# Kernel tuning notes

Measured on AMD Instinct MI355X. Metric: run time of the kernel, lower is better.

## Reference

```python
import jax, jax.numpy as jnp
import numpy as np

SR = 48000.0


def _lin_interp(x, n):
    # Matches torch F.interpolate(mode='linear', align_corners=False) on last axis.
    T = x.shape[-1]
    pos = (jnp.arange(n, dtype=jnp.float32) + 0.5) * (T / n) - 0.5
    pos = jnp.clip(pos, 0.0, T - 1)
    i0 = jnp.floor(pos).astype(jnp.int32)
    i1 = jnp.minimum(i0 + 1, T - 1)
    w = (pos - i0.astype(jnp.float32)).astype(x.dtype)
    return jnp.take(x, i0, axis=-1) * (1.0 - w) + jnp.take(x, i1, axis=-1) * w


def setup_inputs() -> dict:
    key = jax.random.key(0)
    k1, k2, k3 = jax.random.split(key, 3)
    B, T, N = 16, 250, 100
    harm_amps = jax.random.uniform(k1, (B, T, N), dtype=jnp.float32)
    # realistic fundamental frequencies: 80..480 Hz
    f0_hz = 80.0 + 400.0 * jax.random.uniform(k2, (B, T), dtype=jnp.float32)
    # small inharmonicity coefficients (piano-like): ~0..1e-4
    inh = 1e-4 * jax.random.uniform(k3, (B,), dtype=jnp.float32)
    return {"harm_amps": harm_amps, "f0_hz": f0_hz, "inh": inh, "n_samples": 48000}


def reference(harm_amps, f0_hz, inh, n_samples):
    B, T, N = harm_amps.shape
    # upsample amplitudes (B,N,n_samples) and f0 (B,n_samples)
    a = _lin_interp(jnp.transpose(harm_amps, (0, 2, 1)), n_samples)
    f0_up = _lin_interp(f0_hz, n_samples)
    k = jnp.arange(1, N + 1, dtype=jnp.float32)  # harmonic numbers 1..N
    stretch = jnp.sqrt(1.0 + inh[:, None] * k ** 2)  # (B,N)
    inst_freq = f0_up[:, None, :] * (k[None, :] * stretch)[:, :, None]  # (B,N,n)
    nyq_mask = (inst_freq < SR * 0.45).astype(a.dtype)
    phase = jnp.cumsum(2.0 * jnp.pi * inst_freq / SR, axis=-1)
    signal = jnp.sum(a * nyq_mask * jnp.sin(phase), axis=1, keepdims=True)  # (B,1,n)
    return signal / N
```

## Files before the change

### kernel.cpp

```cpp
#include <hip/hip_runtime.h>
#include <cmath>

#pragma clang fp contract(off)

#define SRF   48000.0f
#define NYQF  21600.0f
constexpr float  TWO_PI_F  = 6.283185307179586476925286766559f;
constexpr double INV_2PI_D = 0.15915494309189533576888376337251;
constexpr float  RC1 = (float)INV_2PI_D;
constexpr float  RC2 = (float)(INV_2PI_D - (double)RC1);
constexpr double INV_SR_D = 1.0 / 48000.0;
constexpr float  DD1 = (float)INV_SR_D;
constexpr float  DD2 = (float)(INV_SR_D - (double)DD1);

__device__ __forceinline__ float hsin_rev(float r) {
#if __has_builtin(__builtin_amdgcn_sinf)
    return __builtin_amdgcn_sinf(r);
#else
    return __sinf(r * TWO_PI_F);
#endif
}

__device__ __forceinline__ float div48000(float t) {
    float h = t * DD1;
    float r = __builtin_fmaf(t, DD1, -h);
    float s = __builtin_fmaf(t, DD2, r);
    return h + s;
}

__device__ __forceinline__ float sin_phase(float ph) {
    float h  = ph * RC1;
    float r  = __builtin_fmaf(ph, RC1, -h);
    float s  = __builtin_fmaf(ph, RC2, r);
    float nn = __builtin_rintf(h);
    float fr = (h - nn) + s;
    return hsin_rev(fr);
}

template <int IDX>
__device__ __forceinline__ float grp4_bcast(float v, int lb) {
#if __has_builtin(__builtin_amdgcn_ds_swizzle)
    constexpr int imm = (IDX << 5) | 0x1C;
    return __int_as_float(__builtin_amdgcn_ds_swizzle(__float_as_int(v), imm));
#else
    return __shfl(v, lb + IDX);
#endif
}

__device__ __forceinline__ float kcval(int k, float ib) {
    float kf = (float)(k + 1);
    float k2 = kf * kf;
    float m  = ib * k2;
    float s1 = 1.0f + m;
    float st = (float)sqrt((double)s1);
    return kf * st;
}

__global__ void __launch_bounds__(256) k_f0up(const float* __restrict__ f0,
        float* __restrict__ f0up, float* __restrict__ out,
        int T, int n, float pf) {
    int j = blockIdx.x * 256 + threadIdx.x;
    int b = blockIdx.y;
    if (j >= n) return;
    float pos = ((float)j + 0.5f);
    pos = pos * pf;
    pos = pos - 0.5f;
    pos = fmaxf(pos, 0.0f);
    pos = fminf(pos, (float)(T - 1));
    int   i0 = (int)pos;
    int   i1 = min(i0 + 1, T - 1);
    float w  = pos - (float)i0;
    float omw = 1.0f - w;
    const float* fb = f0 + b * T;
    f0up[(size_t)b * n + j] = fb[i0] * omw + fb[i1] * w;
    out[(size_t)b * n + j]  = 0.0f;
}

__global__ void __launch_bounds__(256) k_scan4(const float* __restrict__ f0up,
        const float* __restrict__ inh, float* __restrict__ scan4,
        int N, int n) {
    __shared__ float lv[6016];
    const int k   = blockIdx.x;
    const int b   = blockIdx.y;
    const int tid = threadIdx.x;
    const float kc = kcval(k, inh[b]);
    const float4* f4 = (const float4*)(f0up + (size_t)b * n);
    const int len4 = n >> 4;

    auto l2of = [&](float4 v) -> float {
        float a0 = div48000(TWO_PI_F * (kc * v.x));
        float a1 = div48000(TWO_PI_F * (kc * v.y));
        float a2 = div48000(TWO_PI_F * (kc * v.z));
        float a3 = div48000(TWO_PI_F * (kc * v.w));
        return (a0 + a1) + (a2 + a3);
    };
    for (int i = tid; i < len4; i += 256) {
        float s01 = l2of(f4[4*i])     + l2of(f4[4*i + 1]);
        float s23 = l2of(f4[4*i + 2]) + l2of(f4[4*i + 3]);
        lv[i] = s01 + s23;
    }
    __syncthreads();

    int offp = 0, lenp = len4, P = 4;
    for (int l = 5; ; ++l) {
        int lenc = lenp >> 1;
        int offc = offp + lenp;
        for (int i = tid; i < lenc; i += 256)
            lv[offc + i] = lv[offp + 2*i] + lv[offp + 2*i + 1];
        __syncthreads();
        P = l;
        if (lenc == 1) break;
        offp = offc; lenp = lenc;
    }
    for (int l = P - 1; l >= 4; --l) {
        int lenl = n >> l;
        int offl = 0;
        for (int m = 4; m < l; ++m) offl += (n >> m);
        int offh = offl + lenl;
        int lenh = n >> (l + 1);
        float*       arr = lv + offl;
        const float* hi  = lv + offh;
        for (int i = tid; i < lenh; i += 256) {
            float v = hi[i];
            int e = 2*i + 2;
            if (e < lenl) arr[e] = v + arr[e];
            arr[2*i + 1] = v;
        }
        __syncthreads();
    }
    float* sp = scan4 + (size_t)(b * N + k) * (len4 + 1);
    if (tid == 0) sp[0] = 0.0f;
    for (int i = tid; i < len4; i += 256) sp[1 + i] = lv[i];
}

__global__ void __launch_bounds__(256) k_synth4(
        const float* __restrict__ harm, const float* __restrict__ f0up,
        const float* __restrict__ inh,  const float* __restrict__ scan4,
        float* __restrict__ out, int B, int T, int N, int n, float pf, int kpg) {
    const int tid  = threadIdx.x;
    const int b    = blockIdx.y;
    const int k0   = blockIdx.z * kpg;
    const int g    = blockIdx.x * 256 + tid;
    const int q    = g >> 2;
    const int c    = g & 3;
    const int NG   = n >> 4;
    const int NGP  = NG + 1;
    const int kend = min(k0 + kpg, N);
    const int kact = kend - k0;
    const bool valid = q < NG;

    __shared__ float2 amps[8 * 32];
    __shared__ float  kcs[32];

    const float ib    = inh[b];
    const float tmaxf = (float)(T - 1);
    for (int i = tid; i < kact; i += 256) kcs[i] = kcval(k0 + i, ib);

    const int j0blk = blockIdx.x * 1024;
    int i0min;
    {
        float p = ((float)j0blk + 0.5f);
        p = p * pf; p = p - 0.5f;
        p = fmaxf(p, 0.0f); p = fminf(p, tmaxf);
        i0min = (int)p;
    }
    for (int idx = tid; idx < 8 * kact; idx += 256) {
        int r = idx / kact, kk = idx - r * kact;
        int r0 = min(i0min + r, T - 1);
        int r1 = min(i0min + r + 1, T - 1);
        float a0 = harm[((size_t)b * T + r0) * N + (k0 + kk)];
        float a1 = harm[((size_t)b * T + r1) * N + (k0 + kk)];
        amps[idx] = make_float2(a0, a1 - a0);
    }
    __syncthreads();

    float u0=0.f,u1=0.f,u2=0.f,u3=0.f;
    float w0=0.f,w1=0.f,w2=0.f,w3=0.f;
    int   a0o=0,a1o=0,a2o=0,a3o=0;
    float um = __builtin_inff();
    if (valid) {
        const float4 v = *(const float4*)(f0up + (size_t)b * n + (size_t)q * 16 + c * 4);
        u0=v.x; u1=v.y; u2=v.z; u3=v.w;
        um = fminf(fminf(u0,u1), fminf(u2,u3));
        const int jb = q * 16 + c * 4;
        #pragma unroll
        for (int i = 0; i < 4; ++i) {
            float p = ((float)(jb + i) + 0.5f);
            p = p * pf; p = p - 0.5f;
            p = fmaxf(p, 0.0f); p = fminf(p, tmaxf);
            int i0 = (int)p;
            float wv = p - (float)i0;
            int aoo  = (i0 - i0min) * kact;
            if (i==0){w0=wv;a0o=aoo;}
            else if (i==1){w1=wv;a1o=aoo;}
            else if (i==2){w2=wv;a2o=aoo;}
            else {w3=wv;a3o=aoo;}
        }
    }
    #pragma unroll
    for (int off = 32; off > 0; off >>= 1)
        um = fminf(um, __shfl_xor(um, off));
    const float umin = um;
    const int lb = (tid & 63) & ~3;

    if (valid) {
        float acc0=0.f, acc1=0.f, acc2=0.f, acc3=0.f;
        const float* s4k = scan4 + (size_t)(b * N + k0) * NGP;
        float g0c = s4k[q];
        float g1c = s4k[q + 1];

        for (int k = k0; k < kend; ++k) {
            const int   kk = k - k0;
            const float kc = kcs[kk];
            if (kc * umin >= NYQF) break;
            const float G0 = g0c, G1 = g1c;
            if (k + 1 < kend) {
                const float* nx = s4k + NGP;
                g0c = nx[q];
                g1c = nx[q + 1];
                s4k = nx;
            }

            float x0 = div48000(TWO_PI_F * (kc * u0));
            float x1 = div48000(TWO_PI_F * (kc * u1));
            float x2 = div48000(TWO_PI_F * (kc * u2));
            float x3 = div48000(TWO_PI_F * (kc * u3));
            float L1p = x0 + x1, L1q = x2 + x3;
            float L2  = L1p + L1q;

            float s0 = grp4_bcast<0>(L2, lb);
            float s1 = grp4_bcast<1>(L2, lb);
            float s2 = grp4_bcast<2>(L2, lb);
            float t01 = s0 + s1;
            float b1v = G0 + s0;
            float b2v = G0 + t01;
            float b3v = b2v + s2;
            float base = (c == 0) ? G0  : (c == 1) ? b1v : (c == 2) ? b2v : b3v;
            float bn   = (c == 0) ? b1v : (c == 1) ? b2v : (c == 2) ? b3v : G1;

            float ph0 = base + x0;
            float ph1 = base + L1p;
            float ph2 = ph1 + x2;
            float ph3 = bn;

            {   float t1 = kc * u0;
                if (t1 < NYQF) { float sv = sin_phase(ph0);
                    float2 a = amps[a0o + kk];
                    acc0 = __builtin_fmaf(__builtin_fmaf(w0, a.y, a.x), sv, acc0); } }
            {   float t1 = kc * u1;
                if (t1 < NYQF) { float sv = sin_phase(ph1);
                    float2 a = amps[a1o + kk];
                    acc1 = __builtin_fmaf(__builtin_fmaf(w1, a.y, a.x), sv, acc1); } }
            {   float t1 = kc * u2;
                if (t1 < NYQF) { float sv = sin_phase(ph2);
                    float2 a = amps[a2o + kk];
                    acc2 = __builtin_fmaf(__builtin_fmaf(w2, a.y, a.x), sv, acc2); } }
            {   float t1 = kc * u3;
                if (t1 < NYQF) { float sv = sin_phase(ph3);
                    float2 a = amps[a3o + kk];
                    acc3 = __builtin_fmaf(__builtin_fmaf(w3, a.y, a.x), sv, acc3); } }
        }

        const float Nf = (float)N;
        float* ob = out + (size_t)b * n + (size_t)q * 16 + c * 4;
        atomicAdd(&ob[0], acc0 / Nf);
        atomicAdd(&ob[1], acc1 / Nf);
        atomicAdd(&ob[2], acc2 / Nf);
        atomicAdd(&ob[3], acc3 / Nf);
    }
}

__global__ void __launch_bounds__(256) k_scan_synth(
        const float* __restrict__ harm, const float* __restrict__ f0up,
        const float* __restrict__ inh,  float* __restrict__ out,
        int B, int T, int N, int n, float pf) {
    extern __shared__ float lv[];
    const int k   = blockIdx.x;
    const int b   = blockIdx.y;
    const int tid = threadIdx.x;
    const float kc = kcval(k, inh[b]);
    const float* fb = f0up + (size_t)b * n;

    auto inc = [&](int j) -> float {
        float u    = fb[j];
        float inst = kc * u;
        float tt   = TWO_PI_F * inst;
        return tt / SRF;
    };

    const int len1 = n >> 1;
    {
        const float4* f4 = (const float4*)fb;
        for (int i = tid; i < (n >> 2); i += 256) {
            float4 u = f4[i];
            float a0 = (TWO_PI_F * (kc * u.x)) / SRF;
            float a1 = (TWO_PI_F * (kc * u.y)) / SRF;
            float a2 = (TWO_PI_F * (kc * u.z)) / SRF;
            float a3 = (TWO_PI_F * (kc * u.w)) / SRF;
            lv[i] = (a0 + a1) + (a2 + a3);
        }
    }
    __syncthreads();
    int offp = 0, lenp = n >> 2, P = 2;
    for (int l = 3; ; ++l) {
        int lenc = lenp >> 1;
        int offc = offp + lenp;
        for (int i = tid; i < lenc; i += 256)
            lv[offc + i] = lv[offp + 2*i] + lv[offp + 2*i + 1];
        __syncthreads();
        P = l;
        if (lenc == 1) break;
        offp = offc; lenp = lenc;
    }
    for (int l = P - 1; l >= 2; --l) {
        int lenl = n >> l;
        int offl = 0;
        for (int m = 2; m < l; ++m) offl += (n >> m);
        float*       arr = lv + offl;
        const float* hi  = lv + offl + lenl;
        int lenh = n >> (l + 1);
        for (int i = tid; i < lenh; i += 256) {
            float v = hi[i];
            int e = 2*i + 2;
            if (e < lenl) arr[e] = v + arr[e];
            arr[2*i + 1] = v;
        }
        __syncthreads();
    }
    const float* scan2 = lv;

    const float  tmaxf = (float)(T - 1);
    const float  invN  = 1.0f / (float)N;
    const float* hb    = harm + (size_t)b * T * N + k;
    float*       ob    = out + (size_t)b * n;

    auto emit = [&](int j, float ph) {
        float u    = fb[j];
        float inst = kc * u;
        if (!(inst < NYQF)) return;
        double pr = (double)ph * INV_2PI_D;
        double fr = pr - rint(pr);
        float  sv = hsin_rev((float)fr);
        float pos = ((float)j + 0.5f);
        pos = pos * pf; pos = pos - 0.5f;
        pos = fmaxf(pos, 0.0f); pos = fminf(pos, tmaxf);
        int   i0 = (int)pos;
        int   i1 = min(i0 + 1, T - 1);
        float w  = pos - (float)i0;
        float a  = hb[(size_t)i0 * N] * (1.0f - w) + hb[(size_t)i1 * N] * w;
        atomicAdd(&ob[j], (a * sv) * invN);
    };

    if (tid == 0) emit(0, inc(0));
    for (int tt = tid; tt < len1; tt += 256) {
        float s1;
        if (tt == 0)      s1 = inc(0) + inc(1);
        else if (tt & 1)  s1 = scan2[(tt - 1) >> 1];
        else              s1 = scan2[(tt >> 1) - 1] + (inc(2*tt) + inc(2*tt + 1));
        emit(2*tt + 1, s1);
        int je = 2*tt + 2;
        if (je < n) emit(je, s1 + inc(je));
    }
}

extern "C" void kernel_launch(void* const* d_in, const int* in_sizes, int n_in,
                              void* d_out, int out_size, void* d_ws, size_t ws_size,
                              hipStream_t stream) {
    const int B = in_sizes[2];
    const int T = in_sizes[1] / B;
    const int N = in_sizes[0] / (B * T);
    const int n = out_size / B;
    const float pf = (float)((double)T / (double)n);

    const float* harm = (const float*)d_in[0];
    const float* f0   = (const float*)d_in[1];
    const float* inh  = (const float*)d_in[2];
    float* out  = (float*)d_out;
    float* f0up = (float*)d_ws;

    const int KZ  = 4;
    const int kpg = (N + KZ - 1) / KZ;
    const int NG  = n / 16;
    const size_t needFast = (size_t)B * n * 4 + (size_t)B * N * (NG + 1) * 4;
    const bool fast = (ws_size >= needFast) && (n % 16 == 0) && (kpg <= 32);

    k_f0up<<<dim3((n + 255) / 256, B), 256, 0, stream>>>(f0, f0up, out, T, n, pf);

    if (fast) {
        float* scan4 = (float*)((char*)d_ws + (size_t)B * n * 4);
        k_scan4<<<dim3(N, B), 256, 0, stream>>>(f0up, inh, scan4, N, n);
        const int tiles = (NG * 4 + 255) / 256;
        k_synth4<<<dim3(tiles, B, KZ), 256, 0, stream>>>(
            harm, f0up, inh, scan4, out, B, T, N, n, pf, kpg);
    } else {
        const size_t lds_bytes = (size_t)(n / 2) * sizeof(float);
        k_scan_synth<<<dim3(N, B), 256, lds_bytes, stream>>>(
            harm, f0up, inh, out, B, T, N, n, pf);
    }
}
```

Before: 153.0 us.

## Process eight samples per thread in synth kernel with pairwise phase broadcast

The synthesis kernel now has each thread handle 8 consecutive samples instead of 4, so a 16-sample group is split across 2 lanes rather than 4. The intra-group phase prefix needs only one even-lane swizzle broadcast instead of three, and per-sample Nyquist branches become predicated selects. Each block now covers 2048 samples with a larger amplitude tile in shared memory, and a host-side guard keeps that tile within bounds. The trade-off is more registers per thread and half as many threads in the grid.

```diff
diff --git a/kernel.cpp b/kernel.cpp
--- a/kernel.cpp
+++ b/kernel.cpp
@@ -37,13 +37,11 @@
     return hsin_rev(fr);
 }
 
-template <int IDX>
-__device__ __forceinline__ float grp4_bcast(float v, int lb) {
+__device__ __forceinline__ float pair_bcast_even(float v, int lane) {
 #if __has_builtin(__builtin_amdgcn_ds_swizzle)
-    constexpr int imm = (IDX << 5) | 0x1C;
-    return __int_as_float(__builtin_amdgcn_ds_swizzle(__float_as_int(v), imm));
+    return __int_as_float(__builtin_amdgcn_ds_swizzle(__float_as_int(v), 0x001E));
 #else
-    return __shfl(v, lb + IDX);
+    return __shfl(v, lane & ~1);
 #endif
 }
 
@@ -133,7 +131,7 @@
     for (int i = tid; i < len4; i += 256) sp[1 + i] = lv[i];
 }
 
-__global__ void __launch_bounds__(256) k_synth4(
+__global__ void __launch_bounds__(256) k_synth8(
         const float* __restrict__ harm, const float* __restrict__ f0up,
         const float* __restrict__ inh,  const float* __restrict__ scan4,
         float* __restrict__ out, int B, int T, int N, int n, float pf, int kpg) {
@@ -141,30 +139,31 @@
     const int b    = blockIdx.y;
     const int k0   = blockIdx.z * kpg;
     const int g    = blockIdx.x * 256 + tid;
-    const int q    = g >> 2;
-    const int c    = g & 3;
+    const int p    = g >> 1;
+    const int c    = g & 1;
+    const int lane = tid & 63;
     const int NG   = n >> 4;
     const int NGP  = NG + 1;
     const int kend = min(k0 + kpg, N);
     const int kact = kend - k0;
-    const bool valid = q < NG;
-
-    __shared__ float2 amps[8 * 32];
+    const bool valid = p < NG;
+
+    __shared__ float2 amps[14 * 32];
     __shared__ float  kcs[32];
 
     const float ib    = inh[b];
     const float tmaxf = (float)(T - 1);
     for (int i = tid; i < kact; i += 256) kcs[i] = kcval(k0 + i, ib);
 
-    const int j0blk = blockIdx.x * 1024;
+    const int j0blk = blockIdx.x * 2048;
     int i0min;
     {
-        float p = ((float)j0blk + 0.5f);
-        p = p * pf; p = p - 0.5f;
-        p = fmaxf(p, 0.0f); p = fminf(p, tmaxf);
-        i0min = (int)p;
-    }
-    for (int idx = tid; idx < 8 * kact; idx += 256) {
+        float pq = ((float)j0blk + 0.5f);
+        pq = pq * pf; pq = pq - 0.5f;
+        pq = fmaxf(pq, 0.0f); pq = fminf(pq, tmaxf);
+        i0min = (int)pq;
+    }
+    for (int idx = tid; idx < 14 * kact; idx += 256) {
         int r = idx / kact, kk = idx - r * kact;
         int r0 = min(i0min + r, T - 1);
         int r1 = min(i0min + r + 1, T - 1);
@@ -174,40 +173,38 @@
     }
     __syncthreads();
 
-    float u0=0.f,u1=0.f,u2=0.f,u3=0.f;
-    float w0=0.f,w1=0.f,w2=0.f,w3=0.f;
-    int   a0o=0,a1o=0,a2o=0,a3o=0;
+    const int j0 = p * 16 + c * 8;
+    float u[8], w[8], acc[8];
+    int   aoo[8];
     float um = __builtin_inff();
     if (valid) {
-        const float4 v = *(const float4*)(f0up + (size_t)b * n + (size_t)q * 16 + c * 4);
-        u0=v.x; u1=v.y; u2=v.z; u3=v.w;
-        um = fminf(fminf(u0,u1), fminf(u2,u3));
-        const int jb = q * 16 + c * 4;
+        const float4 va = *(const float4*)(f0up + (size_t)b * n + j0);
+        const float4 vb = *(const float4*)(f0up + (size_t)b * n + j0 + 4);
+        u[0]=va.x; u[1]=va.y; u[2]=va.z; u[3]=va.w;
+        u[4]=vb.x; u[5]=vb.y; u[6]=vb.z; u[7]=vb.w;
+        um = fminf(fminf(fminf(u[0],u[1]), fminf(u[2],u[3])),
+                   fminf(fminf(u[4],u[5]), fminf(u[6],u[7])));
         #pragma unroll
-        for (int i = 0; i < 4; ++i) {
-            float p = ((float)(jb + i) + 0.5f);
-            p = p * pf; p = p - 0.5f;
-            p = fmaxf(p, 0.0f); p = fminf(p, tmaxf);
-            int i0 = (int)p;
-            float wv = p - (float)i0;
-            int aoo  = (i0 - i0min) * kact;
-            if (i==0){w0=wv;a0o=aoo;}
-            else if (i==1){w1=wv;a1o=aoo;}
-            else if (i==2){w2=wv;a2o=aoo;}
-            else {w3=wv;a3o=aoo;}
+        for (int i = 0; i < 8; ++i) {
+            float pq = ((float)(j0 + i) + 0.5f);
+            pq = pq * pf; pq = pq - 0.5f;
+            pq = fmaxf(pq, 0.0f); pq = fminf(pq, tmaxf);
+            int i0 = (int)pq;
+            w[i]   = pq - (float)i0;
+            aoo[i] = (i0 - i0min) * kact;
+            acc[i] = 0.0f;
         }
     }
     #pragma unroll
     for (int off = 32; off > 0; off >>= 1)
         um = fminf(um, __shfl_xor(um, off));
     const float umin = um;
-    const int lb = (tid & 63) & ~3;
+    const float cf   = (float)c;
 
     if (valid) {
-        float acc0=0.f, acc1=0.f, acc2=0.f, acc3=0.f;
         const float* s4k = scan4 + (size_t)(b * N + k0) * NGP;
-        float g0c = s4k[q];
-        float g1c = s4k[q + 1];
+        float g0c = s4k[p];
+        float g1c = s4k[p + 1];
 
         for (int k = k0; k < kend; ++k) {
             const int   kk = k - k0;
@@ -216,57 +213,54 @@
             const float G0 = g0c, G1 = g1c;
             if (k + 1 < kend) {
                 const float* nx = s4k + NGP;
-                g0c = nx[q];
-                g1c = nx[q + 1];
+                g0c = nx[p];
+                g1c = nx[p + 1];
                 s4k = nx;
             }
 
-            float x0 = div48000(TWO_PI_F * (kc * u0));
-            float x1 = div48000(TWO_PI_F * (kc * u1));
-            float x2 = div48000(TWO_PI_F * (kc * u2));
-            float x3 = div48000(TWO_PI_F * (kc * u3));
-            float L1p = x0 + x1, L1q = x2 + x3;
-            float L2  = L1p + L1q;
-
-            float s0 = grp4_bcast<0>(L2, lb);
-            float s1 = grp4_bcast<1>(L2, lb);
-            float s2 = grp4_bcast<2>(L2, lb);
-            float t01 = s0 + s1;
-            float b1v = G0 + s0;
-            float b2v = G0 + t01;
-            float b3v = b2v + s2;
-            float base = (c == 0) ? G0  : (c == 1) ? b1v : (c == 2) ? b2v : b3v;
-            float bn   = (c == 0) ? b1v : (c == 1) ? b2v : (c == 2) ? b3v : G1;
-
-            float ph0 = base + x0;
-            float ph1 = base + L1p;
-            float ph2 = ph1 + x2;
-            float ph3 = bn;
-
-            {   float t1 = kc * u0;
-                if (t1 < NYQF) { float sv = sin_phase(ph0);
-                    float2 a = amps[a0o + kk];
-                    acc0 = __builtin_fmaf(__builtin_fmaf(w0, a.y, a.x), sv, acc0); } }
-            {   float t1 = kc * u1;
-                if (t1 < NYQF) { float sv = sin_phase(ph1);
-                    float2 a = amps[a1o + kk];
-                    acc1 = __builtin_fmaf(__builtin_fmaf(w1, a.y, a.x), sv, acc1); } }
-            {   float t1 = kc * u2;
-                if (t1 < NYQF) { float sv = sin_phase(ph2);
-                    float2 a = amps[a2o + kk];
-                    acc2 = __builtin_fmaf(__builtin_fmaf(w2, a.y, a.x), sv, acc2); } }
-            {   float t1 = kc * u3;
-                if (t1 < NYQF) { float sv = sin_phase(ph3);
-                    float2 a = amps[a3o + kk];
-                    acc3 = __builtin_fmaf(__builtin_fmaf(w3, a.y, a.x), sv, acc3); } }
+            float t[8], x[8];
+            #pragma unroll
+            for (int i = 0; i < 8; ++i) {
+                t[i] = kc * u[i];
+                x[i] = div48000(TWO_PI_F * t[i]);
+            }
+            float L1a = x[0] + x[1];
+            float L1b = x[2] + x[3];
+            float L1c = x[4] + x[5];
+            float L1d = x[6] + x[7];
+            float sA  = L1a + L1b;
+            float sB  = L1c + L1d;
+            float tt  = sA + sB;
+            float tr  = pair_bcast_even(tt, lane);
+
+            float B0 = __builtin_fmaf(cf, tr, G0);
+            float B1 = B0 + sA;
+
+            float ph[8];
+            ph[0] = B0 + x[0];
+            ph[1] = B0 + L1a;
+            ph[2] = ph[1] + x[2];
+            ph[3] = B1;
+            ph[4] = B1 + x[4];
+            ph[5] = B1 + L1c;
+            ph[6] = ph[5] + x[6];
+            ph[7] = c ? G1 : (G0 + tt);
+
+            #pragma unroll
+            for (int i = 0; i < 8; ++i) {
+                float  sv  = sin_phase(ph[i]);
+                float2 a   = amps[aoo[i] + kk];
+                float  amp = __builtin_fmaf(w[i], a.y, a.x);
+                float  na  = __builtin_fmaf(amp, sv, acc[i]);
+                acc[i] = (t[i] < NYQF) ? na : acc[i];
+            }
         }
 
         const float Nf = (float)N;
-        float* ob = out + (size_t)b * n + (size_t)q * 16 + c * 4;
-        atomicAdd(&ob[0], acc0 / Nf);
-        atomicAdd(&ob[1], acc1 / Nf);
-        atomicAdd(&ob[2], acc2 / Nf);
-        atomicAdd(&ob[3], acc3 / Nf);
+        float* ob = out + (size_t)b * n + j0;
+        #pragma unroll
+        for (int i = 0; i < 8; ++i)
+            atomicAdd(&ob[i], acc[i] / Nf);
     }
 }
 
@@ -382,15 +376,16 @@
     const int kpg = (N + KZ - 1) / KZ;
     const int NG  = n / 16;
     const size_t needFast = (size_t)B * n * 4 + (size_t)B * N * (NG + 1) * 4;
-    const bool fast = (ws_size >= needFast) && (n % 16 == 0) && (kpg <= 32);
+    const bool fast = (ws_size >= needFast) && (n % 16 == 0) && (kpg <= 32)
+                   && ((2048LL * T) <= 11LL * n);
 
     k_f0up<<<dim3((n + 255) / 256, B), 256, 0, stream>>>(f0, f0up, out, T, n, pf);
 
     if (fast) {
         float* scan4 = (float*)((char*)d_ws + (size_t)B * n * 4);
         k_scan4<<<dim3(N, B), 256, 0, stream>>>(f0up, inh, scan4, N, n);
-        const int tiles = (NG * 4 + 255) / 256;
-        k_synth4<<<dim3(tiles, B, KZ), 256, 0, stream>>>(
+        const int tiles = (n / 8 + 255) / 256;
+        k_synth8<<<dim3(tiles, B, KZ), 256, 0, stream>>>(
             harm, f0up, inh, scan4, out, B, T, N, n, pf, kpg);
     } else {
         const size_t lds_bytes = (size_t)(n / 2) * sizeof(float);
```

Result: slower. 196.1 us (+28.2%).
